# Kernel tuning notes

Hardware: AMD Instinct MI355X
Metric: run time of the kernel (lower is better)

Reference implementation:

```python
import jax, jax.numpy as jnp
import numpy as np

NUM_EXPERTS = 8
CAPACITY_FACTOR = 1.0
MIN_CAPACITY = 4


def setup_inputs() -> dict:
    key = jax.random.key(0)
    k0, k1, k2, k3 = jax.random.split(key, 4)
    B, S, M, F, E = 4, 2048, 2048, 8192, NUM_EXPERTS
    return {
        "hidden_states": jax.random.normal(k0, (B, S, M), jnp.float32),
        "wg": jax.random.normal(k1, (M, E), jnp.float32) * 0.02,
        "w1": jax.random.normal(k2, (E, M, F), jnp.float32) * 0.02,
        "b1": jnp.zeros((E, F), jnp.float32),
        "w2": jax.random.normal(k3, (E, F, M), jnp.float32) * 0.02,
        "b2": jnp.zeros((E, M), jnp.float32),
    }


def reference(hidden_states, wg, w1, b1, w2, b2):
    B, S, M = hidden_states.shape
    E = NUM_EXPERTS
    T = B * S  # total tokens
    x = hidden_states.reshape(T, M)

    # ---- top-1 gating (DeepSpeed top1gating, no noise / no RTS) ----
    logits = x @ wg                                  # [T, E]
    gates = jax.nn.softmax(logits, axis=-1)          # [T, E]
    capacity = max(int(np.ceil(T / E * CAPACITY_FACTOR)), MIN_CAPACITY)

    idx1 = jnp.argmax(gates, axis=1)                 # [T]
    mask1 = jax.nn.one_hot(idx1, E, dtype=gates.dtype)  # [T, E]

    # position of each token within its expert's queue
    locations1 = jnp.cumsum(mask1, axis=0) - 1.0     # [T, E]

    # load-balancing aux loss (computed before capacity drop)
    me = jnp.mean(gates, axis=0)
    ce = jnp.mean(mask1, axis=0)
    l_aux = jnp.sum(me * ce) * E

    # drop tokens beyond capacity
    mask1 = mask1 * (locations1 < capacity).astype(mask1.dtype)
    locations1_s = jnp.sum(locations1 * mask1, axis=1).astype(jnp.int32)  # [T]

    gates1 = gates * mask1                           # [T, E], zero for dropped tokens
    loc_sc = jax.nn.one_hot(locations1_s, capacity, dtype=gates.dtype)    # [T, C]

    combine_weights = jnp.einsum("se,sc->sec", gates1, loc_sc)            # [T, E, C]
    dispatch_mask = (combine_weights > 0).astype(x.dtype)                  # [T, E, C]

    # ---- dispatch -> grouped-GEMM experts -> combine ----
    dispatched = jnp.einsum("sec,sm->ecm", dispatch_mask, x)              # [E, C, M]
    h = jax.nn.gelu(jnp.einsum("ecm,emf->ecf", dispatched, w1) + b1[:, None, :])
    expert_out = jnp.einsum("ecf,efm->ecm", h, w2) + b2[:, None, :]       # [E, C, M]

    out = jnp.einsum("sec,ecm->sm", combine_weights, expert_out)          # [T, M]
    return out.reshape(B, S, M), l_aux
```

## Files before the change

### kernel.cpp

```cpp
#include <hip/hip_runtime.h>
#include <hip/hip_bf16.h>
#include <math.h>

#define T_TOK 8192
#define M_DIM 2048
#define F_DIM 8192
#define E_NUM 8
#define CAP   1024

typedef unsigned short u16;
typedef __attribute__((ext_vector_type(8))) short short8;
typedef __attribute__((ext_vector_type(4))) float f32x4;

__device__ __forceinline__ u16 f2bf(float f){
  unsigned int x = __builtin_bit_cast(unsigned int, f);
  unsigned int lsb = (x >> 16) & 1u;
  x += 0x7fffu + lsb;
  return (u16)(x >> 16);
}
__device__ __forceinline__ unsigned int pack2(float a, float b){
  return (unsigned int)f2bf(a) | ((unsigned int)f2bf(b) << 16);
}

typedef __attribute__((address_space(3))) unsigned int lds_uint;
typedef __attribute__((address_space(1))) const unsigned int g_uint;
__device__ __forceinline__ void gl_lds16(const u16* g, u16* l){
  __builtin_amdgcn_global_load_lds((g_uint*)g, (lds_uint*)l, 16, 0, 0);
}

__device__ __forceinline__ float gelu_tanh(float v){
  float u = 0.7978845608028654f * (v + 0.044715f * v * v * v);
  return 0.5f * v * (1.0f + tanhf(u));
}

__global__ __launch_bounds__(256) void gating_kernel(
    const float* __restrict__ x, const float* __restrict__ wg,
    int* __restrict__ expert_id, float* __restrict__ gate_val,
    float* __restrict__ mepart)
{
  int wave = threadIdx.x >> 6, lane = threadIdx.x & 63;
  int t = blockIdx.x * 4 + wave;
  float acc[8];
  #pragma unroll
  for (int e = 0; e < 8; ++e) acc[e] = 0.f;
  const float* xr = x + (size_t)t * M_DIM;
  for (int i = lane; i < M_DIM; i += 64) {
    float xv = xr[i];
    const float4* wr = (const float4*)(wg + (size_t)i * 8);
    float4 w0 = wr[0], w1v = wr[1];
    acc[0] += xv * w0.x;  acc[1] += xv * w0.y;  acc[2] += xv * w0.z;  acc[3] += xv * w0.w;
    acc[4] += xv * w1v.x; acc[5] += xv * w1v.y; acc[6] += xv * w1v.z; acc[7] += xv * w1v.w;
  }
  #pragma unroll
  for (int off = 32; off; off >>= 1)
    #pragma unroll
    for (int e = 0; e < 8; ++e) acc[e] += __shfl_xor(acc[e], off);

  float mx = acc[0]; int bi = 0;
  #pragma unroll
  for (int e = 1; e < 8; ++e) if (acc[e] > mx) { mx = acc[e]; bi = e; }
  float p[8]; float s = 0.f;
  #pragma unroll
  for (int e = 0; e < 8; ++e) { p[e] = expf(acc[e] - mx); s += p[e]; }
  float inv = 1.f / s;

  __shared__ float pl[4][8];
  if (lane == 0) {
    expert_id[t] = bi;
    gate_val[t] = p[bi] * inv;
    #pragma unroll
    for (int e = 0; e < 8; ++e) pl[wave][e] = p[e] * inv;
  }
  __syncthreads();
  if (threadIdx.x < 8) {
    float m = pl[0][threadIdx.x] + pl[1][threadIdx.x] + pl[2][threadIdx.x] + pl[3][threadIdx.x];
    mepart[blockIdx.x * 8 + threadIdx.x] = m;
  }
}

__global__ __launch_bounds__(1024) void scan_kernel(
    const int* __restrict__ expert_id, const float* __restrict__ gate_val,
    const float* __restrict__ mepart, int nmep,
    int* __restrict__ slot_token, float* __restrict__ slot_gate,
    float* __restrict__ laux_out)
{
  __shared__ int wcnt[16][8];
  __shared__ int base[8];
  __shared__ float red[128][8];
  int tid = threadIdx.x, wave = tid >> 6, lane = tid & 63;
  if (tid < 8) base[tid] = 0;

  int e0 = tid & 7, g = tid >> 3;
  float mesum = 0.f;
  for (int r = g; r < nmep; r += 128) mesum += mepart[r * 8 + e0];
  red[g][e0] = mesum;
  __syncthreads();

  for (int tile = 0; tile < T_TOK / 1024; ++tile) {
    int t = tile * 1024 + tid;
    int e = expert_id[t];
    int lp = 0;
    #pragma unroll
    for (int ee = 0; ee < 8; ++ee) {
      unsigned long long m = __ballot(e == ee);
      if (lane == 0) wcnt[wave][ee] = __popcll(m);
      if (ee == e)   lp = __popcll(m & ((1ull << lane) - 1ull));
    }
    __syncthreads();
    int wp = 0;
    for (int w2 = 0; w2 < wave; ++w2) wp += wcnt[w2][e];
    int pos = base[e] + wp + lp;
    if (pos < CAP) {
      slot_token[e * CAP + pos] = t;
      slot_gate[e * CAP + pos] = gate_val[t];
    }
    __syncthreads();
    if (tid < 8) {
      int s = 0;
      for (int w2 = 0; w2 < 16; ++w2) s += wcnt[w2][tid];
      base[tid] += s;
    }
    __syncthreads();
  }

  if (tid < 8) {
    float me = 0.f;
    for (int r = 0; r < 128; ++r) me += red[r][tid];
    me /= (float)T_TOK;
    float ce = (float)base[tid] / (float)T_TOK;
    red[0][tid] = me * ce;
  }
  __syncthreads();
  if (tid == 0) {
    float s = 0.f;
    for (int e = 0; e < 8; ++e) s += red[0][e];
    *laux_out = s * (float)E_NUM;
  }
}

__global__ __launch_bounds__(256) void transpose_cvt_kernel(
    const float* __restrict__ in, u16* __restrict__ out, int R, int Cc)
{
  __shared__ float tile[64][65];
  size_t off = (size_t)blockIdx.z * R * Cc;
  const float* ine = in + off;
  u16* oute = out + off;
  int r0 = blockIdx.y * 64, c0 = blockIdx.x * 64;
  int tr = threadIdx.x >> 4, tc = threadIdx.x & 15;
  #pragma unroll
  for (int it = 0; it < 4; ++it) {
    float4 v = *(const float4*)&ine[(size_t)(r0 + it * 16 + tr) * Cc + c0 + tc * 4];
    tile[it * 16 + tr][tc * 4 + 0] = v.x;
    tile[it * 16 + tr][tc * 4 + 1] = v.y;
    tile[it * 16 + tr][tc * 4 + 2] = v.z;
    tile[it * 16 + tr][tc * 4 + 3] = v.w;
  }
  __syncthreads();
  int oc = threadIdx.x >> 2, q = threadIdx.x & 3;
  u16 vals[16];
  #pragma unroll
  for (int i = 0; i < 16; ++i) vals[i] = f2bf(tile[q * 16 + i][oc]);
  unsigned int w[8];
  #pragma unroll
  for (int i = 0; i < 8; ++i) w[i] = (unsigned int)vals[2 * i] | ((unsigned int)vals[2 * i + 1] << 16);
  u16* orow = oute + (size_t)(c0 + oc) * R + r0 + q * 16;
  uint4 p0; p0.x = w[0]; p0.y = w[1]; p0.z = w[2]; p0.w = w[3];
  uint4 p1; p1.x = w[4]; p1.y = w[5]; p1.z = w[6]; p1.w = w[7];
  *(uint4*)orow = p0;
  *(uint4*)(orow + 8) = p1;
}

__global__ __launch_bounds__(256) void dispatch_kernel(
    const float* __restrict__ x, const int* __restrict__ slot_token,
    u16* __restrict__ Xe)
{
  int slot = blockIdx.x;
  int t = slot_token[slot];
  int c0 = threadIdx.x * 8;
  uint4 pk;
  if (t < 0) {
    pk.x = pk.y = pk.z = pk.w = 0u;
  } else {
    const float* xr = x + (size_t)t * M_DIM + c0;
    float4 a = *(const float4*)xr;
    float4 b = *(const float4*)(xr + 4);
    pk.x = pack2(a.x, a.y); pk.y = pack2(a.z, a.w);
    pk.z = pack2(b.x, b.y); pk.w = pack2(b.z, b.w);
  }
  *(uint4*)(Xe + (size_t)slot * M_DIM + c0) = pk;
}

template<int MH, int GATE>
__device__ __forceinline__ void do_phase(
    const u16* __restrict__ aReg, const u16* __restrict__ bReg,
    int arow_base, int brow_base,
    short8 (&bfr)[4], f32x4 (&acc)[8][4],
    const u16* __restrict__ smat, u16* sreg, int skt, int skh, int K,
    int sg, int srow, int wave)
{
  short8 af[4];
  if (MH == 0) {
    #pragma unroll
    for (int n2 = 0; n2 < 4; ++n2)
      bfr[n2] = *(const short8*)&bReg[brow_base + n2 * 512];
  }
  #pragma unroll
  for (int m2 = 0; m2 < 4; ++m2)
    af[m2] = *(const short8*)&aReg[arow_base + (MH * 4 + m2) * 512];
  const u16* src = smat + (size_t)skt * 64 + skh * 32 + sg * 8;
  #pragma unroll
  for (int j = 0; j < 2; ++j)
    gl_lds16(src + (size_t)(srow + j * 128) * K, sreg + (j * 512 + (wave << 6)) * 8);
  __builtin_amdgcn_s_barrier();
  asm volatile("s_waitcnt lgkmcnt(0)" ::: "memory");
  __builtin_amdgcn_sched_barrier(0);
  __builtin_amdgcn_s_setprio(1);
  #pragma unroll
  for (int m2 = 0; m2 < 4; ++m2)
    #pragma unroll
    for (int n2 = 0; n2 < 4; ++n2)
      acc[MH * 4 + m2][n2] = __builtin_amdgcn_mfma_f32_16x16x32_bf16(
          af[m2], bfr[n2], acc[MH * 4 + m2][n2], 0, 0, 0);
  __builtin_amdgcn_s_setprio(0);
  if (GATE)
    asm volatile("s_waitcnt vmcnt(6)" ::: "memory");
  __builtin_amdgcn_s_barrier();
}

template<int EPI>
__global__ __launch_bounds__(512, 2) void gemm8_kernel(
    const u16* __restrict__ A,
    const u16* __restrict__ B,
    const float* __restrict__ bias,
    u16* __restrict__ Hout,
    float* __restrict__ Out,
    const int* __restrict__ slot_token, const float* __restrict__ slot_gate,
    int K, int NR)
{
  __shared__ u16 SA[2][2][8192];
  __shared__ u16 SB[2][2][8192];

  int orig = blockIdx.x + gridDim.x * (blockIdx.y + gridDim.y * blockIdx.z);
  int nwg  = gridDim.x * gridDim.y * gridDim.z;
  int swz  = (orig & 7) * (nwg >> 3) + (orig >> 3);
  int gxy  = gridDim.x * gridDim.y;
  int e    = swz / gxy;
  int rem  = swz - e * gxy;
  int by   = rem / gridDim.x;
  int bx   = rem - by * gridDim.x;
  int n0 = bx * 256, m0 = by * 256;

  const u16* Ae = A + (size_t)e * CAP * K + (size_t)m0 * K;
  const u16* Be = B + (size_t)e * NR * K + (size_t)n0 * K;

  int tid = threadIdx.x, wave = tid >> 6, lane = tid & 63;
  int wr = wave >> 2, wc = wave & 3;
  int l15 = lane & 15, g2 = lane >> 4;

  int sg   = (tid & 3) ^ ((tid >> 3) & 3);
  int srow = tid >> 2;
  int rs = (l15 >> 1) & 3;
  int cg = (g2 ^ rs) * 8;
  int arow_base = (wr * 128 + l15) * 32 + cg;
  int brow_base = (wc * 64 + l15) * 32 + cg;

  f32x4 acc[8][4];
  #pragma unroll
  for (int m = 0; m < 8; ++m)
    #pragma unroll
    for (int n = 0; n < 4; ++n)
      acc[m][n] = (f32x4){0.f, 0.f, 0.f, 0.f};
  short8 bfr[4];

  auto stage0 = [&](const u16* mat, u16* region, int kt, int kh) {
    const u16* src = mat + (size_t)kt * 64 + kh * 32 + sg * 8;
    #pragma unroll
    for (int j = 0; j < 2; ++j)
      gl_lds16(src + (size_t)(srow + j * 128) * K, region + (j * 512 + (wave << 6)) * 8);
  };

  int nk = K >> 6, ni = nk >> 1;
  stage0(Be, &SB[0][0][0], 0, 0);
  stage0(Ae, &SA[0][0][0], 0, 0);
  stage0(Be, &SB[0][1][0], 0, 1);
  stage0(Ae, &SA[0][1][0], 0, 1);
  stage0(Be, &SB[1][0][0], 1, 0);
  stage0(Ae, &SA[1][0][0], 1, 0);
  stage0(Be, &SB[1][1][0], 1, 1);
  asm volatile("s_waitcnt vmcnt(6)" ::: "memory");
  __builtin_amdgcn_s_barrier();

  #pragma unroll 1
  for (int i = 0; i < ni; ++i) {
    int t1 = 2 * i + 1;
    int t2 = 2 * i + 2 < nk ? 2 * i + 2 : nk - 1;
    int t3 = 2 * i + 3 < nk ? 2 * i + 3 : nk - 1;
    do_phase<0,0>(&SA[0][0][0], &SB[0][0][0], arow_base, brow_base, bfr, acc,
                  Ae, &SA[1][1][0], t1, 1, K, sg, srow, wave);
    do_phase<1,0>(&SA[0][0][0], &SB[0][0][0], arow_base, brow_base, bfr, acc,
                  Be, &SB[0][0][0], t2, 0, K, sg, srow, wave);
    do_phase<0,0>(&SA[0][1][0], &SB[0][1][0], arow_base, brow_base, bfr, acc,
                  Ae, &SA[0][0][0], t2, 0, K, sg, srow, wave);
    do_phase<1,1>(&SA[0][1][0], &SB[0][1][0], arow_base, brow_base, bfr, acc,
                  Be, &SB[0][1][0], t2, 1, K, sg, srow, wave);
    do_phase<0,0>(&SA[1][0][0], &SB[1][0][0], arow_base, brow_base, bfr, acc,
                  Ae, &SA[0][1][0], t2, 1, K, sg, srow, wave);
    do_phase<1,0>(&SA[1][0][0], &SB[1][0][0], arow_base, brow_base, bfr, acc,
                  Be, &SB[1][0][0], t3, 0, K, sg, srow, wave);
    do_phase<0,0>(&SA[1][1][0], &SB[1][1][0], arow_base, brow_base, bfr, acc,
                  Ae, &SA[1][0][0], t3, 0, K, sg, srow, wave);
    do_phase<1,1>(&SA[1][1][0], &SB[1][1][0], arow_base, brow_base, bfr, acc,
                  Be, &SB[1][1][0], t3, 1, K, sg, srow, wave);
  }

  int wrb = wr * 128, wcb = wc * 64;
  const float* be = bias + (size_t)e * NR + n0;
  if (EPI == 0) {
    #pragma unroll
    for (int wm = 0; wm < 8; ++wm) {
      #pragma unroll
      for (int j = 0; j < 4; ++j) {
        int r = wrb + wm * 16 + g2 * 4 + j;
        size_t rowoff = (size_t)e * CAP * F_DIM + (size_t)(m0 + r) * F_DIM + n0;
        #pragma unroll
        for (int n = 0; n < 4; ++n) {
          int c = wcb + n * 16 + l15;
          float v = acc[wm][n][j] + be[c];
          Hout[rowoff + c] = f2bf(gelu_tanh(v));
        }
      }
    }
  } else {
    #pragma unroll
    for (int wm = 0; wm < 8; ++wm) {
      #pragma unroll
      for (int j = 0; j < 4; ++j) {
        int r = wrb + wm * 16 + g2 * 4 + j;
        int slot = e * CAP + m0 + r;
        int tk = slot_token[slot];
        if (tk >= 0) {
          float gv = slot_gate[slot];
          size_t rowoff = (size_t)tk * M_DIM + n0;
          #pragma unroll
          for (int n = 0; n < 4; ++n) {
            int c = wcb + n * 16 + l15;
            Out[rowoff + c] = gv * (acc[wm][n][j] + be[c]);
          }
        }
      }
    }
  }
}

extern "C" void kernel_launch(void* const* d_in, const int* in_sizes, int n_in,
                              void* d_out, int out_size, void* d_ws, size_t ws_size,
                              hipStream_t stream) {
  const float* x  = (const float*)d_in[0];
  const float* wg = (const float*)d_in[1];
  const float* w1 = (const float*)d_in[2];
  const float* b1 = (const float*)d_in[3];
  const float* w2 = (const float*)d_in[4];
  const float* b2 = (const float*)d_in[5];
  float* out = (float*)d_out;

  char* ws = (char*)d_ws;
  size_t o = 0;
  auto alloc = [&](size_t bytes) -> void* {
    void* p = ws + o;
    o += (bytes + 255) & ~(size_t)255;
    return p;
  };
  u16*   w1T        = (u16*)  alloc((size_t)E_NUM * F_DIM * M_DIM * 2);
  u16*   w2T        = (u16*)  alloc((size_t)E_NUM * M_DIM * F_DIM * 2);
  u16*   h          = (u16*)  alloc((size_t)E_NUM * CAP * F_DIM * 2);
  u16*   Xe         = (u16*)  alloc((size_t)E_NUM * CAP * M_DIM * 2);
  int*   expert_id  = (int*)  alloc(T_TOK * 4);
  float* gate_val   = (float*)alloc(T_TOK * 4);
  int*   slot_token = (int*)  alloc(E_NUM * CAP * 4);
  float* slot_gate  = (float*)alloc(E_NUM * CAP * 4);
  float* mepart     = (float*)alloc(2048 * 8 * 4);

  hipMemsetAsync(d_out, 0, (size_t)out_size * 4, stream);
  hipMemsetAsync(slot_token, 0xFF, E_NUM * CAP * 4, stream);

  gating_kernel<<<T_TOK / 4, 256, 0, stream>>>(x, wg, expert_id, gate_val, mepart);
  scan_kernel<<<1, 1024, 0, stream>>>(expert_id, gate_val, mepart, 2048,
                                      slot_token, slot_gate, out + (out_size - 1));
  transpose_cvt_kernel<<<dim3(128, 32, 8), 256, 0, stream>>>(w1, w1T, 2048, 8192);
  transpose_cvt_kernel<<<dim3(32, 128, 8), 256, 0, stream>>>(w2, w2T, 8192, 2048);
  dispatch_kernel<<<E_NUM * CAP, 256, 0, stream>>>(x, slot_token, Xe);
  gemm8_kernel<0><<<dim3(F_DIM / 256, CAP / 256, E_NUM), 512, 0, stream>>>(
      Xe, w1T, b1, h, nullptr, nullptr, nullptr, M_DIM, F_DIM);
  gemm8_kernel<1><<<dim3(M_DIM / 256, CAP / 256, E_NUM), 512, 0, stream>>>(
      h, w2T, b2, nullptr, out, slot_token, slot_gate, F_DIM, M_DIM);
}
```

Before: 1.045 ms.

## Pre-tile GEMM operands into LDS-ready swizzled blocks for contiguous loads

Weights, dispatched activations and the intermediate H are now written by their producer kernels in a tiled layout: 256-row by 32-column blocks, already XOR-swizzled the way LDS expects. This lets the GEMM's global-to-LDS loads read one contiguous 16KB chunk instead of strided rows. The block-index swizzle that improved L2 locality is removed in favour of plain blockIdx mapping. In exchange, the GELU epilogue writes H as scattered 2-byte stores into the tiled layout, and L2 reuse across workgroups may get worse.

```diff
diff --git a/kernel.cpp b/kernel.cpp
--- a/kernel.cpp
+++ b/kernel.cpp
@@ -31,6 +31,11 @@
 __device__ __forceinline__ float gelu_tanh(float v){
   float u = 0.7978845608028654f * (v + 0.044715f * v * v * v);
   return 0.5f * v * (1.0f + tanhf(u));
+}
+
+__device__ __forceinline__ size_t tiled_off(int e, int n, int k, int nt256, int nkt){
+  return ((((size_t)e * nt256 + (n >> 8)) * nkt + (k >> 6)) * 2 + ((k >> 5) & 1)) * 8192
+         + (size_t)((n & 255) * 32 + ((((k >> 3) & 3) ^ ((n >> 1) & 3)) << 3) + (k & 7));
 }
 
 __global__ __launch_bounds__(256) void gating_kernel(
@@ -142,9 +147,8 @@
     const float* __restrict__ in, u16* __restrict__ out, int R, int Cc)
 {
   __shared__ float tile[64][65];
-  size_t off = (size_t)blockIdx.z * R * Cc;
-  const float* ine = in + off;
-  u16* oute = out + off;
+  int e = blockIdx.z;
+  const float* ine = in + (size_t)e * R * Cc;
   int r0 = blockIdx.y * 64, c0 = blockIdx.x * 64;
   int tr = threadIdx.x >> 4, tc = threadIdx.x & 15;
   #pragma unroll
@@ -156,18 +160,19 @@
     tile[it * 16 + tr][tc * 4 + 3] = v.w;
   }
   __syncthreads();
+  int nt256 = Cc >> 8, nkt = R >> 6;
   int oc = threadIdx.x >> 2, q = threadIdx.x & 3;
+  int n = c0 + oc, k0 = r0 + q * 16;
   u16 vals[16];
   #pragma unroll
   for (int i = 0; i < 16; ++i) vals[i] = f2bf(tile[q * 16 + i][oc]);
   unsigned int w[8];
   #pragma unroll
   for (int i = 0; i < 8; ++i) w[i] = (unsigned int)vals[2 * i] | ((unsigned int)vals[2 * i + 1] << 16);
-  u16* orow = oute + (size_t)(c0 + oc) * R + r0 + q * 16;
-  uint4 p0; p0.x = w[0]; p0.y = w[1]; p0.z = w[2]; p0.w = w[3];
-  uint4 p1; p1.x = w[4]; p1.y = w[5]; p1.z = w[6]; p1.w = w[7];
-  *(uint4*)orow = p0;
-  *(uint4*)(orow + 8) = p1;
+  uint4 pa; pa.x = w[0]; pa.y = w[1]; pa.z = w[2]; pa.w = w[3];
+  uint4 pb; pb.x = w[4]; pb.y = w[5]; pb.z = w[6]; pb.w = w[7];
+  *(uint4*)&out[tiled_off(e, n, k0,     nt256, nkt)] = pa;
+  *(uint4*)&out[tiled_off(e, n, k0 + 8, nt256, nkt)] = pb;
 }
 
 __global__ __launch_bounds__(256) void dispatch_kernel(
@@ -175,19 +180,20 @@
     u16* __restrict__ Xe)
 {
   int slot = blockIdx.x;
+  int e = slot >> 10, c = slot & (CAP - 1);
   int t = slot_token[slot];
-  int c0 = threadIdx.x * 8;
+  int m = threadIdx.x * 8;
   uint4 pk;
   if (t < 0) {
     pk.x = pk.y = pk.z = pk.w = 0u;
   } else {
-    const float* xr = x + (size_t)t * M_DIM + c0;
+    const float* xr = x + (size_t)t * M_DIM + m;
     float4 a = *(const float4*)xr;
     float4 b = *(const float4*)(xr + 4);
     pk.x = pack2(a.x, a.y); pk.y = pack2(a.z, a.w);
     pk.z = pack2(b.x, b.y); pk.w = pack2(b.z, b.w);
   }
-  *(uint4*)(Xe + (size_t)slot * M_DIM + c0) = pk;
+  *(uint4*)&Xe[tiled_off(e, c, m, CAP >> 8, M_DIM >> 6)] = pk;
 }
 
 template<int MH, int GATE>
@@ -195,8 +201,8 @@
     const u16* __restrict__ aReg, const u16* __restrict__ bReg,
     int arow_base, int brow_base,
     short8 (&bfr)[4], f32x4 (&acc)[8][4],
-    const u16* __restrict__ smat, u16* sreg, int skt, int skh, int K,
-    int sg, int srow, int wave)
+    const u16* __restrict__ tb, u16* sreg, int skt, int skh,
+    int tid, int wave)
 {
   short8 af[4];
   if (MH == 0) {
@@ -207,10 +213,10 @@
   #pragma unroll
   for (int m2 = 0; m2 < 4; ++m2)
     af[m2] = *(const short8*)&aReg[arow_base + (MH * 4 + m2) * 512];
-  const u16* src = smat + (size_t)skt * 64 + skh * 32 + sg * 8;
+  const u16* src = tb + ((size_t)(skt * 2 + skh) << 13);
   #pragma unroll
   for (int j = 0; j < 2; ++j)
-    gl_lds16(src + (size_t)(srow + j * 128) * K, sreg + (j * 512 + (wave << 6)) * 8);
+    gl_lds16(src + (size_t)(j * 512 + tid) * 8, sreg + (j * 512 + (wave << 6)) * 8);
   __builtin_amdgcn_s_barrier();
   asm volatile("s_waitcnt lgkmcnt(0)" ::: "memory");
   __builtin_amdgcn_sched_barrier(0);
@@ -240,25 +246,16 @@
   __shared__ u16 SA[2][2][8192];
   __shared__ u16 SB[2][2][8192];
 
-  int orig = blockIdx.x + gridDim.x * (blockIdx.y + gridDim.y * blockIdx.z);
-  int nwg  = gridDim.x * gridDim.y * gridDim.z;
-  int swz  = (orig & 7) * (nwg >> 3) + (orig >> 3);
-  int gxy  = gridDim.x * gridDim.y;
-  int e    = swz / gxy;
-  int rem  = swz - e * gxy;
-  int by   = rem / gridDim.x;
-  int bx   = rem - by * gridDim.x;
-  int n0 = bx * 256, m0 = by * 256;
-
-  const u16* Ae = A + (size_t)e * CAP * K + (size_t)m0 * K;
-  const u16* Be = B + (size_t)e * NR * K + (size_t)n0 * K;
+  int e = blockIdx.z;
+  int n0 = blockIdx.x * 256, m0 = blockIdx.y * 256;
+  int nkt = K >> 6;
+  const u16* Atb = A + (((size_t)(e * (CAP >> 8) + (m0 >> 8)) * nkt) * 2) * 8192;
+  const u16* Btb = B + (((size_t)(e * (NR >> 8) + (n0 >> 8)) * nkt) * 2) * 8192;
 
   int tid = threadIdx.x, wave = tid >> 6, lane = tid & 63;
   int wr = wave >> 2, wc = wave & 3;
   int l15 = lane & 15, g2 = lane >> 4;
 
-  int sg   = (tid & 3) ^ ((tid >> 3) & 3);
-  int srow = tid >> 2;
   int rs = (l15 >> 1) & 3;
   int cg = (g2 ^ rs) * 8;
   int arow_base = (wr * 128 + l15) * 32 + cg;
@@ -272,21 +269,21 @@
       acc[m][n] = (f32x4){0.f, 0.f, 0.f, 0.f};
   short8 bfr[4];
 
-  auto stage0 = [&](const u16* mat, u16* region, int kt, int kh) {
-    const u16* src = mat + (size_t)kt * 64 + kh * 32 + sg * 8;
+  auto stage0 = [&](const u16* tb, u16* region, int kt, int kh) {
+    const u16* src = tb + ((size_t)(kt * 2 + kh) << 13);
     #pragma unroll
     for (int j = 0; j < 2; ++j)
-      gl_lds16(src + (size_t)(srow + j * 128) * K, region + (j * 512 + (wave << 6)) * 8);
+      gl_lds16(src + (size_t)(j * 512 + tid) * 8, region + (j * 512 + (wave << 6)) * 8);
   };
 
   int nk = K >> 6, ni = nk >> 1;
-  stage0(Be, &SB[0][0][0], 0, 0);
-  stage0(Ae, &SA[0][0][0], 0, 0);
-  stage0(Be, &SB[0][1][0], 0, 1);
-  stage0(Ae, &SA[0][1][0], 0, 1);
-  stage0(Be, &SB[1][0][0], 1, 0);
-  stage0(Ae, &SA[1][0][0], 1, 0);
-  stage0(Be, &SB[1][1][0], 1, 1);
+  stage0(Btb, &SB[0][0][0], 0, 0);
+  stage0(Atb, &SA[0][0][0], 0, 0);
+  stage0(Btb, &SB[0][1][0], 0, 1);
+  stage0(Atb, &SA[0][1][0], 0, 1);
+  stage0(Btb, &SB[1][0][0], 1, 0);
+  stage0(Atb, &SA[1][0][0], 1, 0);
+  stage0(Btb, &SB[1][1][0], 1, 1);
   asm volatile("s_waitcnt vmcnt(6)" ::: "memory");
   __builtin_amdgcn_s_barrier();
 
@@ -296,21 +293,21 @@
     int t2 = 2 * i + 2 < nk ? 2 * i + 2 : nk - 1;
     int t3 = 2 * i + 3 < nk ? 2 * i + 3 : nk - 1;
     do_phase<0,0>(&SA[0][0][0], &SB[0][0][0], arow_base, brow_base, bfr, acc,
-                  Ae, &SA[1][1][0], t1, 1, K, sg, srow, wave);
+                  Atb, &SA[1][1][0], t1, 1, tid, wave);
     do_phase<1,0>(&SA[0][0][0], &SB[0][0][0], arow_base, brow_base, bfr, acc,
-                  Be, &SB[0][0][0], t2, 0, K, sg, srow, wave);
+                  Btb, &SB[0][0][0], t2, 0, tid, wave);
     do_phase<0,0>(&SA[0][1][0], &SB[0][1][0], arow_base, brow_base, bfr, acc,
-                  Ae, &SA[0][0][0], t2, 0, K, sg, srow, wave);
+                  Atb, &SA[0][0][0], t2, 0, tid, wave);
     do_phase<1,1>(&SA[0][1][0], &SB[0][1][0], arow_base, brow_base, bfr, acc,
-                  Be, &SB[0][1][0], t2, 1, K, sg, srow, wave);
+                  Btb, &SB[0][1][0], t2, 1, tid, wave);
     do_phase<0,0>(&SA[1][0][0], &SB[1][0][0], arow_base, brow_base, bfr, acc,
-                  Ae, &SA[0][1][0], t2, 1, K, sg, srow, wave);
+                  Atb, &SA[0][1][0], t2, 1, tid, wave);
     do_phase<1,0>(&SA[1][0][0], &SB[1][0][0], arow_base, brow_base, bfr, acc,
-                  Be, &SB[1][0][0], t3, 0, K, sg, srow, wave);
+                  Btb, &SB[1][0][0], t3, 0, tid, wave);
     do_phase<0,0>(&SA[1][1][0], &SB[1][1][0], arow_base, brow_base, bfr, acc,
-                  Ae, &SA[1][0][0], t3, 0, K, sg, srow, wave);
+                  Atb, &SA[1][0][0], t3, 0, tid, wave);
     do_phase<1,1>(&SA[1][1][0], &SB[1][1][0], arow_base, brow_base, bfr, acc,
-                  Be, &SB[1][1][0], t3, 1, K, sg, srow, wave);
+                  Btb, &SB[1][1][0], t3, 1, tid, wave);
   }
 
   int wrb = wr * 128, wcb = wc * 64;
@@ -321,12 +318,11 @@
       #pragma unroll
       for (int j = 0; j < 4; ++j) {
         int r = wrb + wm * 16 + g2 * 4 + j;
-        size_t rowoff = (size_t)e * CAP * F_DIM + (size_t)(m0 + r) * F_DIM + n0;
         #pragma unroll
         for (int n = 0; n < 4; ++n) {
           int c = wcb + n * 16 + l15;
           float v = acc[wm][n][j] + be[c];
-          Hout[rowoff + c] = f2bf(gelu_tanh(v));
+          Hout[tiled_off(e, m0 + r, n0 + c, CAP >> 8, F_DIM >> 6)] = f2bf(gelu_tanh(v));
         }
       }
     }
```

Result: faster. 956.4 us (-8.5%).
